# Kernel tuning notes

Hardware: AMD Instinct MI355X
Metric: run time of the kernel (lower is better)

The kernel has to match this reference:

```python
import jax, jax.numpy as jnp
import numpy as np

N, E, H, XD, ED, YD, L = 10000, 640000, 128, 8, 8, 112, 4
EPS_MSG = 1e-7   # GENConv message eps
EPS_SM = 1e-16   # pyg softmax denom eps
EPS_LN = 1e-5    # layernorm eps


def node_ln(x, g, b):
    # torch.nn.LayerNorm over last dim
    m = x.mean(axis=-1, keepdims=True)
    v = x.var(axis=-1, keepdims=True)
    return (x - m) * jax.lax.rsqrt(v + EPS_LN) * g + b


def graph_ln(x, g, b):
    # pyg LayerNorm mode='graph' (no batch): global mean/std over all nodes+channels
    xc = x - x.mean()
    std = jnp.sqrt((xc * xc).mean())
    return xc / (std + EPS_LN) * g + b


def setup_inputs() -> dict:
    key = jax.random.key(0)
    ks = jax.random.split(key, 10)
    rn = lambda k, s, sc: jax.random.normal(k, s, jnp.float32) * sc
    return {
        "x": jax.random.normal(ks[0], (N, XD), jnp.float32),
        "edge_index": jax.random.randint(ks[1], (2, E), 0, N),
        "edge_attr": jax.random.normal(ks[2], (E, ED), jnp.float32),
        "Wn": rn(ks[3], (XD, H), 0.3), "bn": jnp.zeros((H,), jnp.float32),
        "We": rn(ks[4], (ED, H), 0.3), "be": jnp.zeros((H,), jnp.float32),
        "t": jnp.ones((L,), jnp.float32),
        "W1": rn(ks[5], (L, H, 2 * H), 0.08), "b1": jnp.zeros((L, 2 * H), jnp.float32),
        "g1": jnp.ones((L, 2 * H), jnp.float32), "bt1": jnp.zeros((L, 2 * H), jnp.float32),
        "W2": rn(ks[6], (L, 2 * H, H), 0.08), "b2": jnp.zeros((L, H), jnp.float32),
        "lng": jnp.ones((L, H), jnp.float32), "lnb": jnp.zeros((L, H), jnp.float32),
        "Wout": rn(ks[7], (H, YD), 0.08), "bout": jnp.zeros((YD,), jnp.float32),
    }


def reference(x, edge_index, edge_attr, Wn, bn, We, be, t, W1, b1, g1, bt1,
              W2, b2, lng, lnb, Wout, bout):
    src, dst = edge_index[0], edge_index[1]
    h = x @ Wn + bn                       # [N,H] node encoder
    ea = edge_attr @ We + be              # [E,H] edge encoder

    def gen_conv(h, i):
        msg = jax.nn.relu(h[src] + ea) + EPS_MSG          # [E,H]
        logit = msg * t[i]
        mx = jax.ops.segment_max(logit, dst, num_segments=N)
        ex = jnp.exp(logit - mx[dst])
        den = jax.ops.segment_sum(ex, dst, num_segments=N)
        alpha = ex / (den[dst] + EPS_SM)
        agg = jax.ops.segment_sum(alpha * msg, dst, num_segments=N) + h  # root add
        z = jax.nn.relu(graph_ln(agg @ W1[i] + b1[i], g1[i], bt1[i]))
        return z @ W2[i] + b2[i]

    h = gen_conv(h, 0)                    # first layer: conv only
    for i in range(1, L):                 # res+ blocks (dropout off: eval)
        r = jax.nn.relu(node_ln(h, lng[i], lnb[i]))
        h = h + gen_conv(r, i)
    h = jax.nn.relu(node_ln(h, lng[0], lnb[0]))  # layers[0].act(layers[0].norm(x))
    return h @ Wout + bout
```

## Files before the change

kernel.cpp:

```cpp
#include <hip/hip_runtime.h>
#include <math.h>

#define NN 10000
#define NE 640000
#define H 128
#define H2 256
#define XD 8
#define ED 8
#define YD 112
#define NL 4
#define EPS_MSG 1e-7f
#define EPS_SM 1e-16f
#define EPS_LN 1e-5f
#define TM 8
#define NB1 (NN / TM)
#define TNO 16
#define NBO (NN / TNO)

typedef _Float16 h2 __attribute__((ext_vector_type(2)));

__global__ void hist_k(const int* __restrict__ dst, int* __restrict__ counts) {
    int e = blockIdx.x * 256 + threadIdx.x;
    if (e < NE) atomicAdd(&counts[dst[e]], 1);
}

__global__ void scan_k(const int* __restrict__ counts, int* __restrict__ rowptr) {
    __shared__ int part[1024];
    int tid = threadIdx.x;
    const int CH = (NN + 1023) / 1024;
    int base = tid * CH;
    int s = 0;
    for (int j = 0; j < CH; j++) { int i = base + j; if (i < NN) s += counts[i]; }
    part[tid] = s; __syncthreads();
    for (int off = 1; off < 1024; off <<= 1) {
        int v = (tid >= off) ? part[tid - off] : 0;
        __syncthreads();
        part[tid] += v;
        __syncthreads();
    }
    int run = part[tid] - s;
    for (int j = 0; j < CH; j++) {
        int i = base + j;
        if (i < NN) { rowptr[i] = run; run += counts[i]; }
    }
    if (tid == 1023) rowptr[NN] = run;
}

__global__ void scatter_k(const int* __restrict__ dst, const int* __restrict__ rowptr,
                          int* __restrict__ fill, int* __restrict__ perm) {
    int e = blockIdx.x * 256 + threadIdx.x;
    if (e >= NE) return;
    int d = dst[e];
    int pos = rowptr[d] + atomicAdd(&fill[d], 1);
    perm[pos] = e;
}

__global__ void __launch_bounds__(256) packenc_k(
    const int* __restrict__ perm, const int* __restrict__ src,
    const float* __restrict__ eattr, int* __restrict__ srcs,
    _Float16* __restrict__ eacsr,
    const float* __restrict__ x, const float* __restrict__ Wn,
    const float* __restrict__ bn, float* __restrict__ h) {
    int b = blockIdx.x;
    if (b < 2500) {
        int pos = b * 256 + threadIdx.x;
        int e = perm[pos];
        srcs[pos] = src[e];
        const float4* ein = (const float4*)eattr;
        float4 a = ein[(size_t)e * 2];
        float4 bb = ein[(size_t)e * 2 + 1];
        float4 pk;
        _Float16* pp = (_Float16*)&pk;
        pp[0] = (_Float16)a.x; pp[1] = (_Float16)a.y; pp[2] = (_Float16)a.z; pp[3] = (_Float16)a.w;
        pp[4] = (_Float16)bb.x; pp[5] = (_Float16)bb.y; pp[6] = (_Float16)bb.z; pp[7] = (_Float16)bb.w;
        ((float4*)eacsr)[pos] = pk;
    } else {
        int bb = b - 2500;
        int c = threadIdx.x & 127, ln = threadIdx.x >> 7;
        int n = bb * 2 + ln;
        const float4* xr = (const float4*)(x + (size_t)n * XD);
        float4 x0 = xr[0], x1 = xr[1];
        float acc = bn[c];
        acc = fmaf(x0.x, Wn[0 * H + c], acc); acc = fmaf(x0.y, Wn[1 * H + c], acc);
        acc = fmaf(x0.z, Wn[2 * H + c], acc); acc = fmaf(x0.w, Wn[3 * H + c], acc);
        acc = fmaf(x1.x, Wn[4 * H + c], acc); acc = fmaf(x1.y, Wn[5 * H + c], acc);
        acc = fmaf(x1.z, Wn[6 * H + c], acc); acc = fmaf(x1.w, Wn[7 * H + c], acc);
        h[(size_t)n * H + c] = acc;
    }
}

__global__ void __launch_bounds__(512) ea_mm1_k(
    const float* __restrict__ rin, const int* __restrict__ rowptr,
    const int* __restrict__ srcs, const _Float16* __restrict__ eacsr,
    const float* __restrict__ We, const float* __restrict__ be,
    const float* __restrict__ tptr, int layer,
    const float* __restrict__ W1i, const float* __restrict__ b1i,
    float* __restrict__ y1, float* __restrict__ part) {
    int nb = blockIdx.x, tid = threadIdx.x;
    int n0 = nb * TM;
    __shared__ float a[TM][H];

    {
        int wv = tid >> 6, c = tid & 63;
        int n = n0 + wv;
        h2 wA[4], wB[4];
#pragma unroll
        for (int k = 0; k < 4; k++) {
            wA[k][0] = (_Float16)We[(2 * k) * H + c];
            wA[k][1] = (_Float16)We[(2 * k + 1) * H + c];
            wB[k][0] = (_Float16)We[(2 * k) * H + c + 64];
            wB[k][1] = (_Float16)We[(2 * k + 1) * H + c + 64];
        }
        float becA = be[c], becB = be[c + 64];
        float ts2 = tptr[layer] * 1.44269504088896f;
        int beg = rowptr[n], end = rowptr[n + 1];
        const float* rn0 = rin + (size_t)n * H + c;
        float rvA = rn0[0], rvB = rn0[64];
        float denA = 0.f, numA = 0.f, denB = 0.f, numB = 0.f;
#pragma unroll 4
        for (int j = beg; j < end; ++j) {
            int sn = srcs[j];
            float4 raw = *(const float4*)(eacsr + (size_t)j * ED);
            const h2* ep = (const h2*)&raw;
            const float* hp = rin + (size_t)sn * H + c;
            float hvA = hp[0], hvB = hp[64];
            float pA = __builtin_amdgcn_fdot2(ep[0], wA[0], becA, false);
            pA = __builtin_amdgcn_fdot2(ep[1], wA[1], pA, false);
            pA = __builtin_amdgcn_fdot2(ep[2], wA[2], pA, false);
            pA = __builtin_amdgcn_fdot2(ep[3], wA[3], pA, false);
            float pB = __builtin_amdgcn_fdot2(ep[0], wB[0], becB, false);
            pB = __builtin_amdgcn_fdot2(ep[1], wB[1], pB, false);
            pB = __builtin_amdgcn_fdot2(ep[2], wB[2], pB, false);
            pB = __builtin_amdgcn_fdot2(ep[3], wB[3], pB, false);
            float msgA = fmaxf(hvA + pA, 0.f) + EPS_MSG;
            float msgB = fmaxf(hvB + pB, 0.f) + EPS_MSG;
            float peA = __builtin_amdgcn_exp2f(msgA * ts2);
            float peB = __builtin_amdgcn_exp2f(msgB * ts2);
            denA += peA; numA = fmaf(peA, msgA, numA);
            denB += peB; numB = fmaf(peB, msgB, numB);
        }
        a[wv][c]      = numA / (denA + EPS_SM) + rvA;
        a[wv][c + 64] = numB / (denB + EPS_SM) + rvB;
    }
    __syncthreads();

    int o = tid & 255, half = tid >> 8;
    int rb = half * 4;
    float acc[4];
#pragma unroll
    for (int i = 0; i < 4; i++) acc[i] = 0.f;
    for (int k = 0; k < H; k += 4) {
        float w0 = W1i[k * H2 + o];
        float w1 = W1i[(k + 1) * H2 + o];
        float w2 = W1i[(k + 2) * H2 + o];
        float w3 = W1i[(k + 3) * H2 + o];
#pragma unroll
        for (int i = 0; i < 4; i++) {
            float4 av = *(const float4*)&a[rb + i][k];
            acc[i] = fmaf(av.x, w0, acc[i]);
            acc[i] = fmaf(av.y, w1, acc[i]);
            acc[i] = fmaf(av.z, w2, acc[i]);
            acc[i] = fmaf(av.w, w3, acc[i]);
        }
    }
    float bo = b1i[o];
    float ps = 0.f, ps2 = 0.f;
#pragma unroll
    for (int i = 0; i < 4; i++) {
        float v = acc[i] + bo;
        y1[(size_t)(n0 + rb + i) * H2 + o] = v;
        ps += v; ps2 += v * v;
    }
#pragma unroll
    for (int off = 32; off; off >>= 1) { ps += __shfl_xor(ps, off); ps2 += __shfl_xor(ps2, off); }
    __shared__ float red[16];
    int w8 = tid >> 6;
    if ((tid & 63) == 0) { red[w8] = ps; red[8 + w8] = ps2; }
    __syncthreads();
    if (tid == 0) {
        float S = 0.f, S2 = 0.f;
#pragma unroll
        for (int i = 0; i < 8; i++) { S += red[i]; S2 += red[8 + i]; }
        part[nb * 2] = S;
        part[nb * 2 + 1] = S2;
    }
}

__global__ void __launch_bounds__(256) mm2_k(const float* __restrict__ y1,
    const float* __restrict__ g1i, const float* __restrict__ bt1i,
    const float* __restrict__ W2i, const float* __restrict__ b2i,
    const float* __restrict__ part, float* __restrict__ h,
    const float* __restrict__ lgp, const float* __restrict__ lbp,
    float* __restrict__ r, int first) {
    int nb = blockIdx.x, tid = threadIdx.x;
    int o = tid & 127, half = tid >> 7;
    int rb = half * 4;
    int n0 = nb * TM;
    float s = 0.f, s2 = 0.f;
    for (int i = tid; i < NB1; i += 256) { s += part[2 * i]; s2 += part[2 * i + 1]; }
#pragma unroll
    for (int off = 32; off; off >>= 1) { s += __shfl_xor(s, off); s2 += __shfl_xor(s2, off); }
    __shared__ float sred[8];
    int w4 = tid >> 6;
    if ((tid & 63) == 0) { sred[w4] = s; sred[4 + w4] = s2; }
    __syncthreads();
    const float M = (float)NN * (float)H2;
    float m = (sred[0] + sred[1] + sred[2] + sred[3]) / M;
    float var = fmaxf((sred[4] + sred[5] + sred[6] + sred[7]) / M - m * m, 0.f);
    float istd = 1.f / (sqrtf(var) + EPS_LN);

    __shared__ float z[TM][H2];
    __syncthreads();
    {
        const float4* y4 = (const float4*)(y1 + (size_t)n0 * H2);
        const float4* g4 = (const float4*)g1i;
        const float4* b4 = (const float4*)bt1i;
        float4* z4 = (float4*)z;
#pragma unroll
        for (int t = tid; t < TM * H2 / 4; t += 256) {
            int k4 = t & 63;
            float4 v = y4[t];
            float4 g = g4[k4], b = b4[k4];
            v.x = fmaxf((v.x - m) * istd * g.x + b.x, 0.f);
            v.y = fmaxf((v.y - m) * istd * g.y + b.y, 0.f);
            v.z = fmaxf((v.z - m) * istd * g.z + b.z, 0.f);
            v.w = fmaxf((v.w - m) * istd * g.w + b.w, 0.f);
            z4[t] = v;
        }
    }
    __syncthreads();
    float acc[4];
#pragma unroll
    for (int i = 0; i < 4; i++) acc[i] = 0.f;
    for (int k = 0; k < H2; k += 4) {
        float w0 = W2i[k * H + o];
        float w1 = W2i[(k + 1) * H + o];
        float w2 = W2i[(k + 2) * H + o];
        float w3 = W2i[(k + 3) * H + o];
#pragma unroll
        for (int i = 0; i < 4; i++) {
            float4 zv = *(const float4*)&z[rb + i][k];
            acc[i] = fmaf(zv.x, w0, acc[i]);
            acc[i] = fmaf(zv.y, w1, acc[i]);
            acc[i] = fmaf(zv.z, w2, acc[i]);
            acc[i] = fmaf(zv.w, w3, acc[i]);
        }
    }
    float bo = b2i[o];
    float vv[4];
#pragma unroll
    for (int i = 0; i < 4; i++) {
        size_t idx = (size_t)(n0 + rb + i) * H + o;
        float v = acc[i] + bo;
        if (!first) v += h[idx];
        h[idx] = v;
        vv[i] = v;
    }
    __shared__ float rs[2][2][4], rs2[2][2][4];
    int w2i_ = (tid >> 6) & 1;
#pragma unroll
    for (int i = 0; i < 4; i++) {
        float ss = vv[i], ss2 = vv[i] * vv[i];
#pragma unroll
        for (int off = 32; off; off >>= 1) { ss += __shfl_xor(ss, off); ss2 += __shfl_xor(ss2, off); }
        if ((tid & 63) == 0) { rs[half][w2i_][i] = ss; rs2[half][w2i_][i] = ss2; }
    }
    __syncthreads();
    float gc = lgp[o], bc = lbp[o];
#pragma unroll
    for (int i = 0; i < 4; i++) {
        float S = rs[half][0][i] + rs[half][1][i];
        float S2 = rs2[half][0][i] + rs2[half][1][i];
        float mn = S * (1.f / H);
        float vr = S2 * (1.f / H) - mn * mn;
        float inv = rsqrtf(vr + EPS_LN);
        float ov = (vv[i] - mn) * inv * gc + bc;
        r[(size_t)(n0 + rb + i) * H + o] = fmaxf(ov, 0.f);
    }
}

__global__ void __launch_bounds__(128) mmout_k(const float* __restrict__ r,
    const float* __restrict__ Wout, const float* __restrict__ bout,
    float* __restrict__ out) {
    int nb = blockIdx.x, o = threadIdx.x;
    int n0 = nb * TNO;
    __shared__ float a[TNO][H];
    {
        const float4* r4 = (const float4*)(r + (size_t)n0 * H);
        float4* a4 = (float4*)a;
        for (int t = o; t < TNO * H / 4; t += 128) a4[t] = r4[t];
    }
    __syncthreads();
    if (o < YD) {
        float acc[TNO];
#pragma unroll
        for (int i = 0; i < TNO; i++) acc[i] = 0.f;
        for (int k = 0; k < H; k += 4) {
            float w0 = Wout[k * YD + o];
            float w1 = Wout[(k + 1) * YD + o];
            float w2 = Wout[(k + 2) * YD + o];
            float w3 = Wout[(k + 3) * YD + o];
#pragma unroll
            for (int i = 0; i < TNO; i++) {
                float4 av = *(const float4*)&a[i][k];
                acc[i] = fmaf(av.x, w0, acc[i]);
                acc[i] = fmaf(av.y, w1, acc[i]);
                acc[i] = fmaf(av.z, w2, acc[i]);
                acc[i] = fmaf(av.w, w3, acc[i]);
            }
        }
        float bo = bout[o];
#pragma unroll
        for (int i = 0; i < TNO; i++) out[(size_t)(n0 + i) * YD + o] = acc[i] + bo;
    }
}

extern "C" void kernel_launch(void* const* d_in, const int* in_sizes, int n_in,
                              void* d_out, int out_size, void* d_ws, size_t ws_size,
                              hipStream_t stream) {
    const float* x    = (const float*)d_in[0];
    const int*   ei   = (const int*)d_in[1];
    const float* eattr= (const float*)d_in[2];
    const float* Wn   = (const float*)d_in[3];
    const float* bn   = (const float*)d_in[4];
    const float* We   = (const float*)d_in[5];
    const float* be   = (const float*)d_in[6];
    const float* t    = (const float*)d_in[7];
    const float* W1   = (const float*)d_in[8];
    const float* b1   = (const float*)d_in[9];
    const float* g1   = (const float*)d_in[10];
    const float* bt1  = (const float*)d_in[11];
    const float* W2   = (const float*)d_in[12];
    const float* b2   = (const float*)d_in[13];
    const float* lng  = (const float*)d_in[14];
    const float* lnb  = (const float*)d_in[15];
    const float* Wout = (const float*)d_in[16];
    const float* bout = (const float*)d_in[17];
    float* out = (float*)d_out;

    const int* src = ei;
    const int* dst = ei + NE;

    char* ws = (char*)d_ws;
    size_t off = 0;
    auto alloc = [&](size_t bytes) -> char* {
        char* p = ws + off;
        off += (bytes + 255) & ~(size_t)255;
        return p;
    };
    int*      counts = (int*)alloc((size_t)NN * 2 * 4);
    int*      fill   = counts + NN;
    int*      rowptr = (int*)alloc((size_t)(NN + 1) * 4);
    int*      perm   = (int*)alloc((size_t)NE * 4);
    int*      srcs   = (int*)alloc((size_t)NE * 4);
    _Float16* eacsr  = (_Float16*)alloc((size_t)NE * ED * 2);
    float*    h      = (float*)alloc((size_t)NN * H * 4);
    float*    r      = (float*)alloc((size_t)NN * H * 4);
    float*    y1     = (float*)alloc((size_t)NN * H2 * 4);
    float*    part   = (float*)alloc((size_t)NB1 * 2 * 4);
    (void)ws_size; (void)in_sizes; (void)n_in; (void)out_size;

    hipMemsetAsync(counts, 0, (size_t)NN * 2 * 4, stream);

    hist_k<<<(NE + 255) / 256, 256, 0, stream>>>(dst, counts);
    scan_k<<<1, 1024, 0, stream>>>(counts, rowptr);
    scatter_k<<<(NE + 255) / 256, 256, 0, stream>>>(dst, rowptr, fill, perm);
    packenc_k<<<2500 + NN / 2, 256, 0, stream>>>(perm, src, eattr, srcs, eacsr,
                                                 x, Wn, bn, h);

    for (int i = 0; i < NL; i++) {
        const float* cin = (i == 0) ? h : r;
        ea_mm1_k<<<NB1, 512, 0, stream>>>(cin, rowptr, srcs, eacsr, We, be, t, i,
                                          W1 + (size_t)i * H * H2, b1 + i * H2, y1, part);
        int nx = (i == NL - 1) ? 0 : (i + 1);
        mm2_k<<<NB1, 256, 0, stream>>>(y1, g1 + i * H2, bt1 + i * H2,
                                       W2 + (size_t)i * H2 * H, b2 + i * H, part, h,
                                       lng + nx * H, lnb + nx * H, r, (i == 0) ? 1 : 0);
    }
    mmout_k<<<NBO, 128, 0, stream>>>(r, Wout, bout, out);
}
```

Before: 487.4 us.

## Fuse all GENConv layers and output projection into one cooperative persistent kernel

Replaces the per-layer ea_mm1/mm2 launches and the output matmul with a single cooperative kernel that loops over layers, using grid.sync between the aggregation+mm1 phase and the graph-LN+mm2 phase. Tiles shrink to 4 nodes per block of 256 threads, and each lane now handles two adjacent channels with float2 gathers. The goal is to remove kernel launch gaps and tail effects. In exchange it adds grid-wide barriers and a grid sized by occupancy (up to 8 blocks per CU times 256), and the smaller tiles reduce reuse of the W1/W2 weights per load.

```diff
diff --git a/kernel.cpp b/kernel.cpp
--- a/kernel.cpp
+++ b/kernel.cpp
@@ -1,5 +1,8 @@
 #include <hip/hip_runtime.h>
+#include <hip/hip_cooperative_groups.h>
 #include <math.h>
+
+namespace cg = cooperative_groups;
 
 #define NN 10000
 #define NE 640000
@@ -12,10 +15,10 @@
 #define EPS_MSG 1e-7f
 #define EPS_SM 1e-16f
 #define EPS_LN 1e-5f
-#define TM 8
-#define NB1 (NN / TM)
-#define TNO 16
-#define NBO (NN / TNO)
+#define TML 4
+#define NTL (NN / TML)
+#define TMO 8
+#define NTO (NN / TMO)
 
 typedef _Float16 h2 __attribute__((ext_vector_type(2)));
 
@@ -89,229 +92,239 @@
     }
 }
 
-__global__ void __launch_bounds__(512) ea_mm1_k(
-    const float* __restrict__ rin, const int* __restrict__ rowptr,
-    const int* __restrict__ srcs, const _Float16* __restrict__ eacsr,
+__global__ void __launch_bounds__(256, 4) layers_k(
+    float* __restrict__ h, float* __restrict__ r,
+    float* __restrict__ y1, float* __restrict__ part,
+    const int* __restrict__ rowptr, const int* __restrict__ srcs,
+    const _Float16* __restrict__ eacsr,
     const float* __restrict__ We, const float* __restrict__ be,
-    const float* __restrict__ tptr, int layer,
-    const float* __restrict__ W1i, const float* __restrict__ b1i,
-    float* __restrict__ y1, float* __restrict__ part) {
-    int nb = blockIdx.x, tid = threadIdx.x;
-    int n0 = nb * TM;
-    __shared__ float a[TM][H];
-
-    {
-        int wv = tid >> 6, c = tid & 63;
-        int n = n0 + wv;
-        h2 wA[4], wB[4];
-#pragma unroll
-        for (int k = 0; k < 4; k++) {
-            wA[k][0] = (_Float16)We[(2 * k) * H + c];
-            wA[k][1] = (_Float16)We[(2 * k + 1) * H + c];
-            wB[k][0] = (_Float16)We[(2 * k) * H + c + 64];
-            wB[k][1] = (_Float16)We[(2 * k + 1) * H + c + 64];
-        }
-        float becA = be[c], becB = be[c + 64];
-        float ts2 = tptr[layer] * 1.44269504088896f;
-        int beg = rowptr[n], end = rowptr[n + 1];
-        const float* rn0 = rin + (size_t)n * H + c;
-        float rvA = rn0[0], rvB = rn0[64];
-        float denA = 0.f, numA = 0.f, denB = 0.f, numB = 0.f;
-#pragma unroll 4
-        for (int j = beg; j < end; ++j) {
-            int sn = srcs[j];
-            float4 raw = *(const float4*)(eacsr + (size_t)j * ED);
-            const h2* ep = (const h2*)&raw;
-            const float* hp = rin + (size_t)sn * H + c;
-            float hvA = hp[0], hvB = hp[64];
-            float pA = __builtin_amdgcn_fdot2(ep[0], wA[0], becA, false);
-            pA = __builtin_amdgcn_fdot2(ep[1], wA[1], pA, false);
-            pA = __builtin_amdgcn_fdot2(ep[2], wA[2], pA, false);
-            pA = __builtin_amdgcn_fdot2(ep[3], wA[3], pA, false);
-            float pB = __builtin_amdgcn_fdot2(ep[0], wB[0], becB, false);
-            pB = __builtin_amdgcn_fdot2(ep[1], wB[1], pB, false);
-            pB = __builtin_amdgcn_fdot2(ep[2], wB[2], pB, false);
-            pB = __builtin_amdgcn_fdot2(ep[3], wB[3], pB, false);
-            float msgA = fmaxf(hvA + pA, 0.f) + EPS_MSG;
-            float msgB = fmaxf(hvB + pB, 0.f) + EPS_MSG;
-            float peA = __builtin_amdgcn_exp2f(msgA * ts2);
-            float peB = __builtin_amdgcn_exp2f(msgB * ts2);
-            denA += peA; numA = fmaf(peA, msgA, numA);
-            denB += peB; numB = fmaf(peB, msgB, numB);
-        }
-        a[wv][c]      = numA / (denA + EPS_SM) + rvA;
-        a[wv][c + 64] = numB / (denB + EPS_SM) + rvB;
-    }
-    __syncthreads();
-
-    int o = tid & 255, half = tid >> 8;
-    int rb = half * 4;
-    float acc[4];
-#pragma unroll
-    for (int i = 0; i < 4; i++) acc[i] = 0.f;
-    for (int k = 0; k < H; k += 4) {
-        float w0 = W1i[k * H2 + o];
-        float w1 = W1i[(k + 1) * H2 + o];
-        float w2 = W1i[(k + 2) * H2 + o];
-        float w3 = W1i[(k + 3) * H2 + o];
-#pragma unroll
-        for (int i = 0; i < 4; i++) {
-            float4 av = *(const float4*)&a[rb + i][k];
-            acc[i] = fmaf(av.x, w0, acc[i]);
-            acc[i] = fmaf(av.y, w1, acc[i]);
-            acc[i] = fmaf(av.z, w2, acc[i]);
-            acc[i] = fmaf(av.w, w3, acc[i]);
-        }
-    }
-    float bo = b1i[o];
-    float ps = 0.f, ps2 = 0.f;
-#pragma unroll
-    for (int i = 0; i < 4; i++) {
-        float v = acc[i] + bo;
-        y1[(size_t)(n0 + rb + i) * H2 + o] = v;
-        ps += v; ps2 += v * v;
-    }
-#pragma unroll
-    for (int off = 32; off; off >>= 1) { ps += __shfl_xor(ps, off); ps2 += __shfl_xor(ps2, off); }
-    __shared__ float red[16];
-    int w8 = tid >> 6;
-    if ((tid & 63) == 0) { red[w8] = ps; red[8 + w8] = ps2; }
-    __syncthreads();
-    if (tid == 0) {
-        float S = 0.f, S2 = 0.f;
-#pragma unroll
-        for (int i = 0; i < 8; i++) { S += red[i]; S2 += red[8 + i]; }
-        part[nb * 2] = S;
-        part[nb * 2 + 1] = S2;
-    }
-}
-
-__global__ void __launch_bounds__(256) mm2_k(const float* __restrict__ y1,
-    const float* __restrict__ g1i, const float* __restrict__ bt1i,
-    const float* __restrict__ W2i, const float* __restrict__ b2i,
-    const float* __restrict__ part, float* __restrict__ h,
-    const float* __restrict__ lgp, const float* __restrict__ lbp,
-    float* __restrict__ r, int first) {
-    int nb = blockIdx.x, tid = threadIdx.x;
-    int o = tid & 127, half = tid >> 7;
-    int rb = half * 4;
-    int n0 = nb * TM;
-    float s = 0.f, s2 = 0.f;
-    for (int i = tid; i < NB1; i += 256) { s += part[2 * i]; s2 += part[2 * i + 1]; }
-#pragma unroll
-    for (int off = 32; off; off >>= 1) { s += __shfl_xor(s, off); s2 += __shfl_xor(s2, off); }
-    __shared__ float sred[8];
-    int w4 = tid >> 6;
-    if ((tid & 63) == 0) { sred[w4] = s; sred[4 + w4] = s2; }
-    __syncthreads();
-    const float M = (float)NN * (float)H2;
-    float m = (sred[0] + sred[1] + sred[2] + sred[3]) / M;
-    float var = fmaxf((sred[4] + sred[5] + sred[6] + sred[7]) / M - m * m, 0.f);
-    float istd = 1.f / (sqrtf(var) + EPS_LN);
-
-    __shared__ float z[TM][H2];
-    __syncthreads();
-    {
-        const float4* y4 = (const float4*)(y1 + (size_t)n0 * H2);
-        const float4* g4 = (const float4*)g1i;
-        const float4* b4 = (const float4*)bt1i;
-        float4* z4 = (float4*)z;
-#pragma unroll
-        for (int t = tid; t < TM * H2 / 4; t += 256) {
-            int k4 = t & 63;
-            float4 v = y4[t];
-            float4 g = g4[k4], b = b4[k4];
-            v.x = fmaxf((v.x - m) * istd * g.x + b.x, 0.f);
-            v.y = fmaxf((v.y - m) * istd * g.y + b.y, 0.f);
-            v.z = fmaxf((v.z - m) * istd * g.z + b.z, 0.f);
-            v.w = fmaxf((v.w - m) * istd * g.w + b.w, 0.f);
-            z4[t] = v;
-        }
-    }
-    __syncthreads();
-    float acc[4];
-#pragma unroll
-    for (int i = 0; i < 4; i++) acc[i] = 0.f;
-    for (int k = 0; k < H2; k += 4) {
-        float w0 = W2i[k * H + o];
-        float w1 = W2i[(k + 1) * H + o];
-        float w2 = W2i[(k + 2) * H + o];
-        float w3 = W2i[(k + 3) * H + o];
-#pragma unroll
-        for (int i = 0; i < 4; i++) {
-            float4 zv = *(const float4*)&z[rb + i][k];
-            acc[i] = fmaf(zv.x, w0, acc[i]);
-            acc[i] = fmaf(zv.y, w1, acc[i]);
-            acc[i] = fmaf(zv.z, w2, acc[i]);
-            acc[i] = fmaf(zv.w, w3, acc[i]);
-        }
-    }
-    float bo = b2i[o];
-    float vv[4];
-#pragma unroll
-    for (int i = 0; i < 4; i++) {
-        size_t idx = (size_t)(n0 + rb + i) * H + o;
-        float v = acc[i] + bo;
-        if (!first) v += h[idx];
-        h[idx] = v;
-        vv[i] = v;
-    }
-    __shared__ float rs[2][2][4], rs2[2][2][4];
-    int w2i_ = (tid >> 6) & 1;
-#pragma unroll
-    for (int i = 0; i < 4; i++) {
-        float ss = vv[i], ss2 = vv[i] * vv[i];
-#pragma unroll
-        for (int off = 32; off; off >>= 1) { ss += __shfl_xor(ss, off); ss2 += __shfl_xor(ss2, off); }
-        if ((tid & 63) == 0) { rs[half][w2i_][i] = ss; rs2[half][w2i_][i] = ss2; }
-    }
-    __syncthreads();
-    float gc = lgp[o], bc = lbp[o];
-#pragma unroll
-    for (int i = 0; i < 4; i++) {
-        float S = rs[half][0][i] + rs[half][1][i];
-        float S2 = rs2[half][0][i] + rs2[half][1][i];
-        float mn = S * (1.f / H);
-        float vr = S2 * (1.f / H) - mn * mn;
-        float inv = rsqrtf(vr + EPS_LN);
-        float ov = (vv[i] - mn) * inv * gc + bc;
-        r[(size_t)(n0 + rb + i) * H + o] = fmaxf(ov, 0.f);
-    }
-}
-
-__global__ void __launch_bounds__(128) mmout_k(const float* __restrict__ r,
+    const float* __restrict__ tptr,
+    const float* __restrict__ W1, const float* __restrict__ b1,
+    const float* __restrict__ g1, const float* __restrict__ bt1,
+    const float* __restrict__ W2, const float* __restrict__ b2,
+    const float* __restrict__ lng, const float* __restrict__ lnb,
     const float* __restrict__ Wout, const float* __restrict__ bout,
     float* __restrict__ out) {
-    int nb = blockIdx.x, o = threadIdx.x;
-    int n0 = nb * TNO;
-    __shared__ float a[TNO][H];
+    cg::grid_group grid = cg::this_grid();
+    const int tid = threadIdx.x;
+    const int G = gridDim.x;
+    __shared__ float smem[TML * H2];
+    __shared__ float red[4], red2[4];
+    __shared__ float rs[2][2][2], rs2b[2][2][2];
+
+    const int wv = tid >> 6, l = tid & 63;
+    const int c0 = 2 * l;
+    h2 wA[4], wB[4];
+#pragma unroll
+    for (int k = 0; k < 4; k++) {
+        wA[k][0] = (_Float16)We[(2 * k) * H + c0];
+        wA[k][1] = (_Float16)We[(2 * k + 1) * H + c0];
+        wB[k][0] = (_Float16)We[(2 * k) * H + c0 + 1];
+        wB[k][1] = (_Float16)We[(2 * k + 1) * H + c0 + 1];
+    }
+    const float becA = be[c0], becB = be[c0 + 1];
+
+    for (int li = 0; li < NL; ++li) {
+        const float* cin = (li == 0) ? h : r;
+        const float* W1i = W1 + (size_t)li * H * H2;
+        const float* b1i = b1 + (size_t)li * H2;
+        const float ts2 = tptr[li] * 1.44269504088896f;
+
+        for (int tile = blockIdx.x; tile < NTL; tile += G) {
+            int n0 = tile * TML;
+            __syncthreads();
+            {
+                int n = n0 + wv;
+                int beg = __builtin_amdgcn_readfirstlane(rowptr[n]);
+                int end = __builtin_amdgcn_readfirstlane(rowptr[n + 1]);
+                const float2 rv = *(const float2*)(cin + (size_t)n * H + c0);
+                float denA = 0.f, numA = 0.f, denB = 0.f, numB = 0.f;
+#pragma unroll 4
+                for (int j = beg; j < end; ++j) {
+                    int sn = srcs[j];
+                    float4 raw = *(const float4*)(eacsr + (size_t)j * ED);
+                    const h2* ep = (const h2*)&raw;
+                    float2 hv = *(const float2*)(cin + (size_t)sn * H + c0);
+                    float pA = __builtin_amdgcn_fdot2(ep[0], wA[0], becA, false);
+                    pA = __builtin_amdgcn_fdot2(ep[1], wA[1], pA, false);
+                    pA = __builtin_amdgcn_fdot2(ep[2], wA[2], pA, false);
+                    pA = __builtin_amdgcn_fdot2(ep[3], wA[3], pA, false);
+                    float pB = __builtin_amdgcn_fdot2(ep[0], wB[0], becB, false);
+                    pB = __builtin_amdgcn_fdot2(ep[1], wB[1], pB, false);
+                    pB = __builtin_amdgcn_fdot2(ep[2], wB[2], pB, false);
+                    pB = __builtin_amdgcn_fdot2(ep[3], wB[3], pB, false);
+                    float msgA = fmaxf(hv.x + pA, 0.f) + EPS_MSG;
+                    float msgB = fmaxf(hv.y + pB, 0.f) + EPS_MSG;
+                    float peA = __builtin_amdgcn_exp2f(msgA * ts2);
+                    float peB = __builtin_amdgcn_exp2f(msgB * ts2);
+                    denA += peA; numA = fmaf(peA, msgA, numA);
+                    denB += peB; numB = fmaf(peB, msgB, numB);
+                }
+                float2 av;
+                av.x = numA / (denA + EPS_SM) + rv.x;
+                av.y = numB / (denB + EPS_SM) + rv.y;
+                *(float2*)&smem[wv * H + c0] = av;
+            }
+            __syncthreads();
+            int o = tid;
+            float acc[TML];
+#pragma unroll
+            for (int i = 0; i < TML; i++) acc[i] = 0.f;
+            for (int k = 0; k < H; k += 4) {
+                float w0 = W1i[k * H2 + o];
+                float w1 = W1i[(k + 1) * H2 + o];
+                float w2 = W1i[(k + 2) * H2 + o];
+                float w3 = W1i[(k + 3) * H2 + o];
+#pragma unroll
+                for (int i = 0; i < TML; i++) {
+                    float4 av = *(const float4*)&smem[i * H + k];
+                    acc[i] = fmaf(av.x, w0, acc[i]);
+                    acc[i] = fmaf(av.y, w1, acc[i]);
+                    acc[i] = fmaf(av.z, w2, acc[i]);
+                    acc[i] = fmaf(av.w, w3, acc[i]);
+                }
+            }
+            float bo = b1i[o];
+            float ps = 0.f, ps2 = 0.f;
+#pragma unroll
+            for (int i = 0; i < TML; i++) {
+                float v = acc[i] + bo;
+                y1[(size_t)(n0 + i) * H2 + o] = v;
+                ps += v; ps2 += v * v;
+            }
+#pragma unroll
+            for (int off = 32; off; off >>= 1) { ps += __shfl_xor(ps, off); ps2 += __shfl_xor(ps2, off); }
+            if ((tid & 63) == 0) { red[wv] = ps; red2[wv] = ps2; }
+            __syncthreads();
+            if (tid == 0) {
+                part[tile * 2]     = red[0] + red[1] + red[2] + red[3];
+                part[tile * 2 + 1] = red2[0] + red2[1] + red2[2] + red2[3];
+            }
+        }
+        grid.sync();
+
+        float s = 0.f, s2 = 0.f;
+        for (int i2 = tid; i2 < NTL; i2 += 256) { s += part[2 * i2]; s2 += part[2 * i2 + 1]; }
+#pragma unroll
+        for (int off = 32; off; off >>= 1) { s += __shfl_xor(s, off); s2 += __shfl_xor(s2, off); }
+        if ((tid & 63) == 0) { red[wv] = s; red2[wv] = s2; }
+        __syncthreads();
+        const float M = (float)NN * (float)H2;
+        float m = (red[0] + red[1] + red[2] + red[3]) / M;
+        float var = fmaxf((red2[0] + red2[1] + red2[2] + red2[3]) / M - m * m, 0.f);
+        float istd = 1.f / (sqrtf(var) + EPS_LN);
+
+        const float* W2i = W2 + (size_t)li * H2 * H;
+        const float* b2i = b2 + (size_t)li * H;
+        const float* g1i = g1 + (size_t)li * H2;
+        const float* bt1i = bt1 + (size_t)li * H2;
+        int nx = (li == NL - 1) ? 0 : (li + 1);
+        const float* lgp = lng + (size_t)nx * H;
+        const float* lbp = lnb + (size_t)nx * H;
+        int first = (li == 0);
+        int o = tid & 127, half = tid >> 7;
+        int rb = half * 2;
+        int w2i = (tid >> 6) & 1;
+        for (int tile = blockIdx.x; tile < NTL; tile += G) {
+            int n0 = tile * TML;
+            __syncthreads();
+            {
+                const float4* y4 = (const float4*)(y1 + (size_t)n0 * H2);
+                const float4* g4 = (const float4*)g1i;
+                const float4* b4 = (const float4*)bt1i;
+                float4* z4 = (float4*)smem;
+                int t2 = tid;
+                int k4 = t2 & 63;
+                float4 v = y4[t2];
+                float4 g = g4[k4], b = b4[k4];
+                v.x = fmaxf((v.x - m) * istd * g.x + b.x, 0.f);
+                v.y = fmaxf((v.y - m) * istd * g.y + b.y, 0.f);
+                v.z = fmaxf((v.z - m) * istd * g.z + b.z, 0.f);
+                v.w = fmaxf((v.w - m) * istd * g.w + b.w, 0.f);
+                z4[t2] = v;
+            }
+            __syncthreads();
+            float acc[2] = {0.f, 0.f};
+            for (int k = 0; k < H2; k += 4) {
+                float w0 = W2i[k * H + o];
+                float w1 = W2i[(k + 1) * H + o];
+                float w2 = W2i[(k + 2) * H + o];
+                float w3 = W2i[(k + 3) * H + o];
+#pragma unroll
+                for (int i = 0; i < 2; i++) {
+                    float4 zv = *(const float4*)&smem[(rb + i) * H2 + k];
+                    acc[i] = fmaf(zv.x, w0, acc[i]);
+                    acc[i] = fmaf(zv.y, w1, acc[i]);
+                    acc[i] = fmaf(zv.z, w2, acc[i]);
+                    acc[i] = fmaf(zv.w, w3, acc[i]);
+                }
+            }
+            float bo = b2i[o];
+            float vv[2];
+#pragma unroll
+            for (int i = 0; i < 2; i++) {
+                size_t idx = (size_t)(n0 + rb + i) * H + o;
+                float v = acc[i] + bo;
+                if (!first) v += h[idx];
+                h[idx] = v;
+                vv[i] = v;
+            }
+#pragma unroll
+            for (int i = 0; i < 2; i++) {
+                float ss = vv[i], ss2 = vv[i] * vv[i];
+#pragma unroll
+                for (int off = 32; off; off >>= 1) { ss += __shfl_xor(ss, off); ss2 += __shfl_xor(ss2, off); }
+                if ((tid & 63) == 0) { rs[half][w2i][i] = ss; rs2b[half][w2i][i] = ss2; }
+            }
+            __syncthreads();
+            float gc = lgp[o], bc = lbp[o];
+#pragma unroll
+            for (int i = 0; i < 2; i++) {
+                float S = rs[half][0][i] + rs[half][1][i];
+                float S2 = rs2b[half][0][i] + rs2b[half][1][i];
+                float mn = S * (1.f / H);
+                float vr = S2 * (1.f / H) - mn * mn;
+                float inv = rsqrtf(vr + EPS_LN);
+                float ov = (vv[i] - mn) * inv * gc + bc;
+                r[(size_t)(n0 + rb + i) * H + o] = fmaxf(ov, 0.f);
+            }
+        }
+        grid.sync();
+    }
+
     {
-        const float4* r4 = (const float4*)(r + (size_t)n0 * H);
-        float4* a4 = (float4*)a;
-        for (int t = o; t < TNO * H / 4; t += 128) a4[t] = r4[t];
-    }
-    __syncthreads();
-    if (o < YD) {
-        float acc[TNO];
-#pragma unroll
-        for (int i = 0; i < TNO; i++) acc[i] = 0.f;
-        for (int k = 0; k < H; k += 4) {
-            float w0 = Wout[k * YD + o];
-            float w1 = Wout[(k + 1) * YD + o];
-            float w2 = Wout[(k + 2) * YD + o];
-            float w3 = Wout[(k + 3) * YD + o];
-#pragma unroll
-            for (int i = 0; i < TNO; i++) {
-                float4 av = *(const float4*)&a[i][k];
-                acc[i] = fmaf(av.x, w0, acc[i]);
-                acc[i] = fmaf(av.y, w1, acc[i]);
-                acc[i] = fmaf(av.z, w2, acc[i]);
-                acc[i] = fmaf(av.w, w3, acc[i]);
+        int o = tid & 127, half = tid >> 7;
+        int rb = half * 4;
+        for (int tile = blockIdx.x; tile < NTO; tile += G) {
+            int n0 = tile * TMO;
+            __syncthreads();
+            {
+                const float4* r4 = (const float4*)(r + (size_t)n0 * H);
+                float4* a4 = (float4*)smem;
+                a4[tid] = r4[tid];
+            }
+            __syncthreads();
+            if (o < YD) {
+                float acc[4] = {0.f, 0.f, 0.f, 0.f};
+                for (int k = 0; k < H; k += 4) {
+                    float w0 = Wout[k * YD + o];
+                    float w1 = Wout[(k + 1) * YD + o];
+                    float w2 = Wout[(k + 2) * YD + o];
+                    float w3 = Wout[(k + 3) * YD + o];
+#pragma unroll
+                    for (int i = 0; i < 4; i++) {
+                        float4 av = *(const float4*)&smem[(rb + i) * H + k];
+                        acc[i] = fmaf(av.x, w0, acc[i]);
+                        acc[i] = fmaf(av.y, w1, acc[i]);
+                        acc[i] = fmaf(av.z, w2, acc[i]);
+                        acc[i] = fmaf(av.w, w3, acc[i]);
+                    }
+                }
+                float bo = bout[o];
+#pragma unroll
+                for (int i = 0; i < 4; i++) out[(size_t)(n0 + rb + i) * YD + o] = acc[i] + bo;
             }
         }
-        float bo = bout[o];
-#pragma unroll
-        for (int i = 0; i < TNO; i++) out[(size_t)(n0 + i) * YD + o] = acc[i] + bo;
     }
 }
 
@@ -357,7 +370,7 @@
     float*    h      = (float*)alloc((size_t)NN * H * 4);
     float*    r      = (float*)alloc((size_t)NN * H * 4);
     float*    y1     = (float*)alloc((size_t)NN * H2 * 4);
-    float*    part   = (float*)alloc((size_t)NB1 * 2 * 4);
+    float*    part   = (float*)alloc((size_t)NTL * 2 * 4);
     (void)ws_size; (void)in_sizes; (void)n_in; (void)out_size;
 
     hipMemsetAsync(counts, 0, (size_t)NN * 2 * 4, stream);
@@ -368,14 +381,20 @@
     packenc_k<<<2500 + NN / 2, 256, 0, stream>>>(perm, src, eattr, srcs, eacsr,
                                                  x, Wn, bn, h);
 
-    for (int i = 0; i < NL; i++) {
-        const float* cin = (i == 0) ? h : r;
-        ea_mm1_k<<<NB1, 512, 0, stream>>>(cin, rowptr, srcs, eacsr, We, be, t, i,
-                                          W1 + (size_t)i * H * H2, b1 + i * H2, y1, part);
-        int nx = (i == NL - 1) ? 0 : (i + 1);
-        mm2_k<<<NB1, 256, 0, stream>>>(y1, g1 + i * H2, bt1 + i * H2,
-                                       W2 + (size_t)i * H2 * H, b2 + i * H, part, h,
-                                       lng + nx * H, lnb + nx * H, r, (i == 0) ? 1 : 0);
-    }
-    mmout_k<<<NBO, 128, 0, stream>>>(r, Wout, bout, out);
-}
+    int occ = 0;
+    hipOccupancyMaxActiveBlocksPerMultiprocessor(&occ, layers_k, 256, 0);
+    if (occ < 1) occ = 1;
+    if (occ > 8) occ = 8;
+    int G = occ * 256;
+    if (G > NTL) G = NTL;
+
+    void* kargs[] = {
+        (void*)&h, (void*)&r, (void*)&y1, (void*)&part,
+        (void*)&rowptr, (void*)&srcs, (void*)&eacsr,
+        (void*)&We, (void*)&be, (void*)&t,
+        (void*)&W1, (void*)&b1, (void*)&g1, (void*)&bt1,
+        (void*)&W2, (void*)&b2, (void*)&lng, (void*)&lnb,
+        (void*)&Wout, (void*)&bout, (void*)&out
+    };
+    hipLaunchCooperativeKernel((void*)layers_k, dim3(G), dim3(256), kargs, 0, stream);
+}
```

Result: slower. 1.300 ms (+166.7%).
